# Optimization experiments

Hardware: AMD Instinct MI355X
Metric: run time of the kernel (lower is better)

Reference implementation:

```python
import jax, jax.numpy as jnp
import numpy as np

S = 4  # MC samples


def _gat_layer(x, mask, w, a_src, a_dst, bias):
    # x: (b,n,fin)  w: (H,fin,fout)  mask: (b,n,n) bool
    h = jnp.einsum('bnf,hfo->bhno', x, w)                      # (b,H,n,fout)
    th = jnp.tanh(h)
    att_src = jnp.einsum('bhno,ho->bhn', th, a_src)
    att_dst = jnp.einsum('bhno,ho->bhn', th, a_dst)
    logits = jax.nn.leaky_relu(att_src[:, :, :, None] + att_dst[:, :, None, :], 0.2)
    logits = jnp.where(mask[:, None, :, :], logits, jnp.float32(-1e9))
    att = jax.nn.softmax(logits, axis=-1)                      # (b,H,n,n)
    out = jnp.einsum('bhij,bhjo->bhio', att, h) + bias         # (b,H,n,fout)
    return out, att


def setup_inputs() -> dict:
    key = jax.random.key(0)
    ks = jax.random.split(key, 11)
    b, n, f0, emb_d = 128, 128, 64, 64
    H1, f1, H2, f2 = 8, 16, 1, 2
    fin1 = f0 + emb_d            # 128 (n_units[0] += 64)
    fin2 = H1 * f1               # 128 (heads concatenated between layers)
    x = jax.random.normal(ks[0], (b, n, f0), jnp.float32)
    emb = jax.random.normal(ks[1], (b, n, emb_d), jnp.float32)
    adj = jax.random.randint(ks[2], (b, n, n), 0, 2).astype(jnp.int32)
    adj = jnp.maximum(adj, jnp.eye(n, dtype=jnp.int32)[None])  # self-loops keep softmax rows valid
    w1 = jax.random.normal(ks[3], (S, H1, fin1, f1), jnp.float32) * 0.1
    a_src1 = jax.random.normal(ks[4], (S, H1, f1), jnp.float32) * 0.1
    a_dst1 = jax.random.normal(ks[5], (S, H1, f1), jnp.float32) * 0.1
    b1 = jax.random.normal(ks[6], (f1,), jnp.float32) * 0.1
    w2 = jax.random.normal(ks[7], (S, H2, fin2, f2), jnp.float32) * 0.1
    a_src2 = jax.random.normal(ks[8], (S, H2, f2), jnp.float32) * 0.1
    a_dst2 = jax.random.normal(ks[9], (S, H2, f2), jnp.float32) * 0.1
    b2 = jax.random.normal(ks[10], (f2,), jnp.float32) * 0.1
    return dict(x=x, emb=emb, adj=adj, w1=w1, a_src1=a_src1, a_dst1=a_dst1, b1=b1,
                w2=w2, a_src2=a_src2, a_dst2=a_dst2, b2=b2)


def reference(x, emb, adj, w1, a_src1, a_dst1, b1, w2, a_src2, a_dst2, b2):
    mask = adj.astype(bool)
    x0 = jnp.concatenate([x, emb], axis=-1)                    # (b,n,128)
    b, n = x0.shape[0], x0.shape[1]
    xs = jnp.broadcast_to(x0, (S,) + x0.shape)                 # same input for each MC sample
    layer = jax.vmap(_gat_layer, in_axes=(0, None, 0, 0, 0, None))
    # layer 1 (per-sample variational weights), ELU activation
    h1, att1 = layer(xs, mask, w1, a_src1, a_dst1, b1)         # h1: (S,b,H1,n,f1)
    h1 = jax.nn.elu(h1)
    # concat heads: transpose(1,2).view(bs,n,-1)
    xs2 = jnp.transpose(h1, (0, 1, 3, 2, 4)).reshape(S, b, n, -1)
    # layer 2 (last layer): no activation, mean over heads
    h2, att2 = layer(xs2, mask, w2, a_src2, a_dst2, b2)        # (S,b,1,n,2)
    out = h2.mean(axis=2)                                      # (S,b,n,2)
    logp = jax.nn.log_softmax(out, axis=-1)[:, :, -1, :]       # (S,b,2) -> ego node
    result = jnp.mean(logp, axis=0)                            # var_mean -> mean (return_uncertainty=False)
    return result
```

## Files before the change

### kernel.cpp

```cpp
#include <hip/hip_runtime.h>
#include <stdint.h>
#include <math.h>

typedef __attribute__((ext_vector_type(8))) short short8;
typedef __attribute__((ext_vector_type(4))) float floatx4;

#define L_HU    0
#define L_BF    32768
#define L_SRC   49152
#define L_DST   53248
#define L_MASK  57344
#define L_RED   59392
#define L_D2    59648
#define L_SIZE  60160

#define WS_MASK_BYTES 262144

union F8 { short8 s8; uint32_t u[4]; };

__device__ __forceinline__ uint32_t packbf(float a, float b){
  uint32_t ua = __float_as_uint(a), ub = __float_as_uint(b);
  uint32_t ra = (ua + 0x7fffu + ((ua>>16)&1u)) >> 16;
  uint32_t rb = (ub + 0x7fffu + ((ub>>16)&1u)) >> 16;
  return ra | (rb<<16);
}
__device__ __forceinline__ float fast_tanh(float x){
  float e = __expf(2.f*x);
  return 1.f - 2.f*__builtin_amdgcn_rcpf(e + 1.f);
}

__global__ void mask_build(const int* __restrict__ adj, uint32_t* __restrict__ mask_ws) {
  const int t = threadIdx.x;
  const int row = blockIdx.x*4 + (t>>6);
  const int lane = t & 63;
  const int* ar = adj + (size_t)row*128;
  uint64_t m0 = __ballot(ar[lane] != 0);
  uint64_t m1 = __ballot(ar[64+lane] != 0);
  if (lane == 0) {
    ((uint4*)mask_ws)[row] = make_uint4((uint32_t)m0, (uint32_t)(m0>>32),
                                        (uint32_t)m1, (uint32_t)(m1>>32));
  }
}

__global__ __launch_bounds__(512,4) void gat_fused(
    const float* __restrict__ x,  const float* __restrict__ emb,
    const float* __restrict__ w1, const float* __restrict__ a_src1,
    const float* __restrict__ a_dst1, const float* __restrict__ b1,
    const float* __restrict__ w2, const float* __restrict__ a_src2,
    const float* __restrict__ a_dst2, const float* __restrict__ b2,
    const uint32_t* __restrict__ mask_ws, float* __restrict__ logp_ws)
{
  __shared__ __align__(16) char smem[L_SIZE];
  uint32_t* h_u   = (uint32_t*)(smem + L_HU);
  uint16_t* h_u16 = (uint16_t*)(smem + L_HU);
  char*     bf_b  = smem + L_BF;
  float2*   h2p   = (float2*)(smem + L_BF);
  float*    src_l = (float*)(smem + L_SRC);
  float*    dst_l = (float*)(smem + L_DST);
  uint32_t* mask_l= (uint32_t*)(smem + L_MASK);
  const uint4* mask4 = (const uint4*)(smem + L_MASK);
  float*    red   = (float*)(smem + L_RED);
  float*    d2_l  = (float*)(smem + L_D2);

  const int t  = threadIdx.x;
  const int s  = blockIdx.x >> 7;
  const int bb = blockIdx.x & 127;
  const int lane = t & 63, w = t >> 6;
  const int of = lane & 15, kg = lane >> 4;

  mask_l[t] = mask_ws[(size_t)bb*512 + t];

  const int arow = w*16 + of;
  const float* xrow = x   + ((size_t)bb*128 + arow)*64;
  const float* erow = emb + ((size_t)bb*128 + arow)*64;
  short8 af[4];
  #pragma unroll
  for (int ks=0; ks<4; ++ks){
    int k = ks*32 + kg*8;
    const float* p = (k<64) ? (xrow+k) : (erow + (k-64));
    float4 f0 = *(const float4*)p, f1 = *(const float4*)(p+4);
    F8 fr;
    fr.u[0]=packbf(f0.x,f0.y); fr.u[1]=packbf(f0.z,f0.w);
    fr.u[2]=packbf(f1.x,f1.y); fr.u[3]=packbf(f1.z,f1.w);
    af[ks]=fr.s8;
  }

  const float* w1s = w1 + (size_t)s*16384;
  floatx4 acc[8];
  #pragma unroll
  for (int ct=0; ct<8; ++ct) acc[ct]=(floatx4){0.f,0.f,0.f,0.f};

  for (int c=0; c<2; ++c){
    if (c) __syncthreads();
    #pragma unroll
    for (int r=0; r<2; ++r){
      int q  = t + r*512;
      int ln = q & 63, ks2 = (q>>6)&1, ct = q>>7;
      int kk = (c*2+ks2)*32 + (ln>>4)*8;
      int oo = ln & 15;
      const float* wp = w1s + ct*2048 + kk*16 + oo;
      float v0=wp[0],  v1=wp[16], v2=wp[32], v3=wp[48];
      float v4=wp[64], v5=wp[80], v6=wp[96], v7=wp[112];
      F8 fr;
      fr.u[0]=packbf(v0,v1); fr.u[1]=packbf(v2,v3);
      fr.u[2]=packbf(v4,v5); fr.u[3]=packbf(v6,v7);
      *(short8*)(bf_b + ((ct*2+ks2)*64 + ln)*16) = fr.s8;
    }
    __syncthreads();
    #pragma unroll
    for (int ct=0; ct<8; ++ct)
      #pragma unroll
      for (int ks2=0; ks2<2; ++ks2){
        short8 bfr = *(const short8*)(bf_b + ((ct*2+ks2)*64 + lane)*16);
        acc[ct] = __builtin_amdgcn_mfma_f32_16x16x32_bf16(af[c*2+ks2], bfr, acc[ct], 0,0,0);
      }
  }

  #pragma unroll
  for (int ct=0; ct<8; ++ct){
    float asv = a_src1[s*128 + ct*16 + of];
    float adv = a_dst1[s*128 + ct*16 + of];
    float ps[4], pd[4];
    #pragma unroll
    for (int r=0; r<4; ++r){
      float th = fast_tanh(acc[ct][r]);
      ps[r] = th*asv; pd[r] = th*adv;
    }
    #pragma unroll
    for (int off=1; off<16; off<<=1)
      #pragma unroll
      for (int r=0; r<4; ++r){ ps[r]+=__shfl_xor(ps[r],off); pd[r]+=__shfl_xor(pd[r],off); }
    if (of==0){
      #pragma unroll
      for (int r=0; r<4; ++r){
        int i = w*16 + kg*4 + r;
        src_l[ct*128+i]=ps[r]; dst_l[ct*128+i]=pd[r];
      }
    }
    #pragma unroll
    for (int r=0; r<4; ++r){
      float pv = __shfl_xor(acc[ct][r],1);
      if ((of&1)==0){
        int i = w*16 + kg*4 + r;
        h_u[i*64 + ct*8 + (of>>1)] = packbf(acc[ct][r], pv);
      }
    }
  }
  __syncthreads();

  const int hd = w;
  float b1v  = b1[of];
  float w2c0 = w2[s*256 + (hd*16+of)*2 + 0];
  float w2c1 = w2[s*256 + (hd*16+of)*2 + 1];
  short8 hb[4];
  #pragma unroll
  for (int ks=0; ks<4; ++ks){
    F8 fr;
    #pragma unroll
    for (int v=0; v<4; ++v){
      int j = ks*32 + kg*8 + 2*v;
      uint32_t lo = h_u16[j*128     + hd*16 + of];
      uint32_t hi = h_u16[(j+1)*128 + hd*16 + of];
      fr.u[v] = lo | (hi<<16);
    }
    hb[ks]=fr.s8;
  }

  for (int rt=0; rt<8; ++rt){
    const int im = rt*16 + of;
    float srcv = src_l[hd*128 + im];
    uint4 mrow = mask4[im];
    floatx4 acc2 = (floatx4){0.f,0.f,0.f,0.f};
    float zp = 0.f;
    #pragma unroll
    for (int ks=0; ks<4; ++ks){
      const float* dp = dst_l + hd*128 + ks*32 + kg*8;
      float4 d0 = *(const float4*)dp, d1 = *(const float4*)(dp+4);
      uint32_t mw = (ks==0)?mrow.x:(ks==1)?mrow.y:(ks==2)?mrow.z:mrow.w;
      uint32_t mbyte = mw >> (kg*8);
      float dj[8] = {d0.x,d0.y,d0.z,d0.w,d1.x,d1.y,d1.z,d1.w};
      float e[8];
      #pragma unroll
      for (int jj=0; jj<8; ++jj){
        float t0 = srcv + dj[jj];
        float lr = fmaxf(t0, 0.2f*t0);
        float ev = __expf(lr);
        ev = ((mbyte>>jj)&1u) ? ev : 0.f;
        e[jj]=ev; zp += ev;
      }
      F8 fr;
      fr.u[0]=packbf(e[0],e[1]); fr.u[1]=packbf(e[2],e[3]);
      fr.u[2]=packbf(e[4],e[5]); fr.u[3]=packbf(e[6],e[7]);
      acc2 = __builtin_amdgcn_mfma_f32_16x16x32_bf16(fr.s8, hb[ks], acc2, 0,0,0);
    }
    float zr = zp + __shfl_xor(zp,16); zr += __shfl_xor(zr,32);
    float zi = __builtin_amdgcn_rcpf(zr);
    float pc0[4], pc1[4];
    #pragma unroll
    for (int r=0; r<4; ++r){
      float ziR = __shfl(zi, kg*4+r);
      float o  = fmaf(acc2[r], ziR, b1v);
      float oe = (o>0.f) ? o : (__expf(o)-1.f);
      pc0[r]=oe*w2c0; pc1[r]=oe*w2c1;
    }
    #pragma unroll
    for (int off=1; off<16; off<<=1)
      #pragma unroll
      for (int r=0; r<4; ++r){ pc0[r]+=__shfl_xor(pc0[r],off); pc1[r]+=__shfl_xor(pc1[r],off); }
    if (of==0){
      #pragma unroll
      for (int r=0; r<4; ++r){
        int i = rt*16 + kg*4 + r;
        h2p[w*128 + i] = make_float2(pc0[r], pc1[r]);
      }
    }
  }
  __syncthreads();

  {
    const int jn = t>>1, cc = t&1;
    const bool act = (t<256);
    float hv=0.f, v=-1e9f;
    if (act){
      #pragma unroll
      for (int ww=0; ww<8; ++ww){
        float2 p = h2p[ww*128+jn];
        hv += cc ? p.y : p.x;
      }
      float th2 = fast_tanh(hv);
      float ps2 = th2*a_src2[s*2+cc];
      float pd2 = th2*a_dst2[s*2+cc];
      ps2 += __shfl_xor(ps2,1);
      pd2 += __shfl_xor(pd2,1);
      if (cc==0) d2_l[jn]=pd2;
      if (t==254) red[40]=ps2;
    }
    __syncthreads();
    if (act){
      float t0 = red[40] + d2_l[jn];
      float lg = fmaxf(t0, 0.2f*t0);
      uint32_t bit = (mask_l[127*4 + (jn>>5)] >> (jn&31)) & 1u;
      v = bit ? lg : -1e9f;
    }
    float mloc = v;
    #pragma unroll
    for (int off=32; off>=1; off>>=1) mloc = fmaxf(mloc, __shfl_xor(mloc,off));
    if (lane==0) red[w]=mloc;
    __syncthreads();
    float M = fmaxf(fmaxf(red[0],red[1]), fmaxf(red[2],red[3]));
    float e2 = act ? __expf(v-M) : 0.f;
    float vA = e2*hv;
    float vZ = (cc==0 && act) ? e2 : 0.f;
    #pragma unroll
    for (int off=2; off<=32; off<<=1){ vA+=__shfl_xor(vA,off); vZ+=__shfl_xor(vZ,off); }
    if (lane==0){ red[8+w]=vA; red[24+w]=vZ; }
    if (lane==1){ red[16+w]=vA; }
    __syncthreads();
    if (t==0){
      float S0 = red[8]+red[9]+red[10]+red[11];
      float S1 = red[16]+red[17]+red[18]+red[19];
      float Z  = red[24]+red[25]+red[26]+red[27];
      float o0 = S0/Z + b2[0];
      float o1 = S1/Z + b2[1];
      float mm = fmaxf(o0,o1);
      float lse = mm + logf(__expf(o0-mm)+__expf(o1-mm));
      logp_ws[(s*128+bb)*2+0] = o0 - lse;
      logp_ws[(s*128+bb)*2+1] = o1 - lse;
    }
  }
}

__global__ void reduce_s(const float* __restrict__ lp, float* __restrict__ out) {
  const int t = threadIdx.x;
  out[t] = 0.25f*(lp[t] + lp[256+t] + lp[512+t] + lp[768+t]);
}

extern "C" void kernel_launch(void* const* d_in, const int* in_sizes, int n_in,
                              void* d_out, int out_size, void* d_ws, size_t ws_size,
                              hipStream_t stream) {
  const float* x      = (const float*)d_in[0];
  const float* emb    = (const float*)d_in[1];
  const int*   adj    = (const int*)d_in[2];
  const float* w1     = (const float*)d_in[3];
  const float* a_src1 = (const float*)d_in[4];
  const float* a_dst1 = (const float*)d_in[5];
  const float* b1     = (const float*)d_in[6];
  const float* w2     = (const float*)d_in[7];
  const float* a_src2 = (const float*)d_in[8];
  const float* a_dst2 = (const float*)d_in[9];
  const float* b2     = (const float*)d_in[10];

  uint32_t* mask_ws = (uint32_t*)d_ws;
  float*    logp_ws = (float*)((char*)d_ws + WS_MASK_BYTES);

  mask_build<<<dim3(4096), dim3(256), 0, stream>>>(adj, mask_ws);
  gat_fused<<<dim3(512), dim3(512), 0, stream>>>(x, emb, w1, a_src1, a_dst1, b1,
                                                 w2, a_src2, a_dst2, b2,
                                                 mask_ws, logp_ws);
  reduce_s<<<dim3(1), dim3(256), 0, stream>>>(logp_ws, (float*)d_out);
}
```

Before: 140.9 us.

## Pre-pack W1 into MFMA fragment layout, fragment-order H staging, atomic S-reduction

W1 is converted to bf16 once, in MFMA B-fragment order, by a merged prep kernel that also builds the adjacency bitmask. The fused kernel then loads its B fragments straight from global memory, dropping the per-block conversion, LDS staging and two barriers. Layer-1 outputs are written to LDS already in layer-2 fragment layout, so each lane rebuilds them with one vector load instead of scattered 16-bit gathers. The final reduce kernel is replaced by a memset plus atomicAdd of 0.25-weighted log-probs, which makes the summation order nondeterministic and adds a memset launch.

```diff
diff --git a/kernel.cpp b/kernel.cpp
--- a/kernel.cpp
+++ b/kernel.cpp
@@ -5,16 +5,17 @@
 typedef __attribute__((ext_vector_type(8))) short short8;
 typedef __attribute__((ext_vector_type(4))) float floatx4;
 
-#define L_HU    0
-#define L_BF    32768
-#define L_SRC   49152
-#define L_DST   53248
-#define L_MASK  57344
-#define L_RED   59392
-#define L_D2    59648
-#define L_SIZE  60160
+#define L_HF    0
+#define L_H2P   32768
+#define L_SRC   40960
+#define L_DST   45056
+#define L_MASK  49152
+#define L_RED   51200
+#define L_D2    51456
+#define L_SIZE  51968
 
 #define WS_MASK_BYTES 262144
+#define WS_W1F_BYTES  131072
 
 union F8 { short8 s8; uint32_t u[4]; };
 
@@ -29,32 +30,48 @@
   return 1.f - 2.f*__builtin_amdgcn_rcpf(e + 1.f);
 }
 
-__global__ void mask_build(const int* __restrict__ adj, uint32_t* __restrict__ mask_ws) {
-  const int t = threadIdx.x;
-  const int row = blockIdx.x*4 + (t>>6);
-  const int lane = t & 63;
-  const int* ar = adj + (size_t)row*128;
-  uint64_t m0 = __ballot(ar[lane] != 0);
-  uint64_t m1 = __ballot(ar[64+lane] != 0);
-  if (lane == 0) {
-    ((uint4*)mask_ws)[row] = make_uint4((uint32_t)m0, (uint32_t)(m0>>32),
-                                        (uint32_t)m1, (uint32_t)(m1>>32));
+__global__ void prep(const int* __restrict__ adj, const float* __restrict__ w1,
+                     uint32_t* __restrict__ mask_ws, uint32_t* __restrict__ w1f) {
+  const int blk = blockIdx.x, t = threadIdx.x;
+  if (blk < 1024) {
+    const int lane = t & 63;
+    const int row0 = blk*16 + (t>>6)*4;
+    #pragma unroll
+    for (int i=0;i<4;++i){
+      const int row = row0 + i;
+      const int* ar = adj + (size_t)row*128;
+      uint64_t m0 = __ballot(ar[lane] != 0);
+      uint64_t m1 = __ballot(ar[64+lane] != 0);
+      if (lane == 0)
+        ((uint4*)mask_ws)[row] = make_uint4((uint32_t)m0,(uint32_t)(m0>>32),
+                                            (uint32_t)m1,(uint32_t)(m1>>32));
+    }
+  } else {
+    const int tid = (blk-1024)*256 + t;
+    const int lane = tid & 63, ks = (tid>>6)&3, ct = (tid>>8)&7, s = tid>>11;
+    const float* wp = w1 + s*16384 + ct*2048 + (ks*32 + (lane>>4)*8)*16 + (lane&15);
+    uint4 u;
+    u.x = packbf(wp[0*16],  wp[1*16]);
+    u.y = packbf(wp[2*16],  wp[3*16]);
+    u.z = packbf(wp[4*16],  wp[5*16]);
+    u.w = packbf(wp[6*16],  wp[7*16]);
+    ((uint4*)w1f)[tid] = u;
   }
 }
 
 __global__ __launch_bounds__(512,4) void gat_fused(
     const float* __restrict__ x,  const float* __restrict__ emb,
-    const float* __restrict__ w1, const float* __restrict__ a_src1,
-    const float* __restrict__ a_dst1, const float* __restrict__ b1,
+    const float* __restrict__ a_src1, const float* __restrict__ a_dst1,
+    const float* __restrict__ b1,
     const float* __restrict__ w2, const float* __restrict__ a_src2,
     const float* __restrict__ a_dst2, const float* __restrict__ b2,
-    const uint32_t* __restrict__ mask_ws, float* __restrict__ logp_ws)
+    const uint32_t* __restrict__ mask_ws, const char* __restrict__ w1f,
+    float* __restrict__ outp)
 {
   __shared__ __align__(16) char smem[L_SIZE];
-  uint32_t* h_u   = (uint32_t*)(smem + L_HU);
-  uint16_t* h_u16 = (uint16_t*)(smem + L_HU);
-  char*     bf_b  = smem + L_BF;
-  float2*   h2p   = (float2*)(smem + L_BF);
+  char*     hf    = smem + L_HF;
+  uint32_t* hf_u  = (uint32_t*)(smem + L_HF);
+  float2*   h2p   = (float2*)(smem + L_H2P);
   float*    src_l = (float*)(smem + L_SRC);
   float*    dst_l = (float*)(smem + L_DST);
   uint32_t* mask_l= (uint32_t*)(smem + L_MASK);
@@ -85,37 +102,19 @@
     af[ks]=fr.s8;
   }
 
-  const float* w1s = w1 + (size_t)s*16384;
+  const char* w1fs = w1f + (size_t)s*32768;
   floatx4 acc[8];
   #pragma unroll
   for (int ct=0; ct<8; ++ct) acc[ct]=(floatx4){0.f,0.f,0.f,0.f};
-
-  for (int c=0; c<2; ++c){
-    if (c) __syncthreads();
-    #pragma unroll
-    for (int r=0; r<2; ++r){
-      int q  = t + r*512;
-      int ln = q & 63, ks2 = (q>>6)&1, ct = q>>7;
-      int kk = (c*2+ks2)*32 + (ln>>4)*8;
-      int oo = ln & 15;
-      const float* wp = w1s + ct*2048 + kk*16 + oo;
-      float v0=wp[0],  v1=wp[16], v2=wp[32], v3=wp[48];
-      float v4=wp[64], v5=wp[80], v6=wp[96], v7=wp[112];
-      F8 fr;
-      fr.u[0]=packbf(v0,v1); fr.u[1]=packbf(v2,v3);
-      fr.u[2]=packbf(v4,v5); fr.u[3]=packbf(v6,v7);
-      *(short8*)(bf_b + ((ct*2+ks2)*64 + ln)*16) = fr.s8;
-    }
-    __syncthreads();
-    #pragma unroll
-    for (int ct=0; ct<8; ++ct)
-      #pragma unroll
-      for (int ks2=0; ks2<2; ++ks2){
-        short8 bfr = *(const short8*)(bf_b + ((ct*2+ks2)*64 + lane)*16);
-        acc[ct] = __builtin_amdgcn_mfma_f32_16x16x32_bf16(af[c*2+ks2], bfr, acc[ct], 0,0,0);
-      }
-  }
-
+  #pragma unroll
+  for (int ct=0; ct<8; ++ct)
+    #pragma unroll
+    for (int ks=0; ks<4; ++ks){
+      short8 bfr = *(const short8*)(w1fs + ((ct*4+ks)*64 + lane)*16);
+      acc[ct] = __builtin_amdgcn_mfma_f32_16x16x32_bf16(af[ks], bfr, acc[ct], 0,0,0);
+    }
+
+  const int ks_h = w>>1, kgp = (w&1)*2 + (kg>>1), vv = (kg&1)*2;
   #pragma unroll
   for (int ct=0; ct<8; ++ct){
     float asv = a_src1[s*128 + ct*16 + of];
@@ -137,14 +136,10 @@
         src_l[ct*128+i]=ps[r]; dst_l[ct*128+i]=pd[r];
       }
     }
-    #pragma unroll
-    for (int r=0; r<4; ++r){
-      float pv = __shfl_xor(acc[ct][r],1);
-      if ((of&1)==0){
-        int i = w*16 + kg*4 + r;
-        h_u[i*64 + ct*8 + (of>>1)] = packbf(acc[ct][r], pv);
-      }
-    }
+    uint32_t p0 = packbf(acc[ct][0], acc[ct][1]);
+    uint32_t p1 = packbf(acc[ct][2], acc[ct][3]);
+    uint32_t* dsth = hf_u + ((ct*4+ks_h)*64 + kgp*16 + of)*4 + vv;
+    *(uint2*)dsth = make_uint2(p0, p1);
   }
   __syncthreads();
 
@@ -154,17 +149,8 @@
   float w2c1 = w2[s*256 + (hd*16+of)*2 + 1];
   short8 hb[4];
   #pragma unroll
-  for (int ks=0; ks<4; ++ks){
-    F8 fr;
-    #pragma unroll
-    for (int v=0; v<4; ++v){
-      int j = ks*32 + kg*8 + 2*v;
-      uint32_t lo = h_u16[j*128     + hd*16 + of];
-      uint32_t hi = h_u16[(j+1)*128 + hd*16 + of];
-      fr.u[v] = lo | (hi<<16);
-    }
-    hb[ks]=fr.s8;
-  }
+  for (int ks=0; ks<4; ++ks)
+    hb[ks] = *(const short8*)(hf + ((hd*4+ks)*64 + lane)*16);
 
   for (int rt=0; rt<8; ++rt){
     const int im = rt*16 + of;
@@ -264,15 +250,10 @@
       float o1 = S1/Z + b2[1];
       float mm = fmaxf(o0,o1);
       float lse = mm + logf(__expf(o0-mm)+__expf(o1-mm));
-      logp_ws[(s*128+bb)*2+0] = o0 - lse;
-      logp_ws[(s*128+bb)*2+1] = o1 - lse;
-    }
-  }
-}
-
-__global__ void reduce_s(const float* __restrict__ lp, float* __restrict__ out) {
-  const int t = threadIdx.x;
-  out[t] = 0.25f*(lp[t] + lp[256+t] + lp[512+t] + lp[768+t]);
+      atomicAdd(outp + bb*2 + 0, 0.25f*(o0 - lse));
+      atomicAdd(outp + bb*2 + 1, 0.25f*(o1 - lse));
+    }
+  }
 }
 
 extern "C" void kernel_launch(void* const* d_in, const int* in_sizes, int n_in,
@@ -291,11 +272,12 @@
   const float* b2     = (const float*)d_in[10];
 
   uint32_t* mask_ws = (uint32_t*)d_ws;
-  float*    logp_ws = (float*)((char*)d_ws + WS_MASK_BYTES);
-
-  mask_build<<<dim3(4096), dim3(256), 0, stream>>>(adj, mask_ws);
-  gat_fused<<<dim3(512), dim3(512), 0, stream>>>(x, emb, w1, a_src1, a_dst1, b1,
+  uint32_t* w1f     = (uint32_t*)((char*)d_ws + WS_MASK_BYTES);
+
+  hipMemsetAsync(d_out, 0, (size_t)out_size*sizeof(float), stream);
+  prep<<<dim3(1056), dim3(256), 0, stream>>>(adj, w1, mask_ws, w1f);
+  gat_fused<<<dim3(512), dim3(512), 0, stream>>>(x, emb, a_src1, a_dst1, b1,
                                                  w2, a_src2, a_dst2, b2,
-                                                 mask_ws, logp_ws);
-  reduce_s<<<dim3(1), dim3(256), 0, stream>>>(logp_ws, (float*)d_out);
-}
+                                                 mask_ws, (const char*)w1f,
+                                                 (float*)d_out);
+}
```

New measurement: 139.8 us. Within noise of the previous version (-0.8%).
